# Kernel tuning notes

Hardware: AMD Instinct MI355X
Metric: run time of the kernel (lower is better)

## Reference

```python
import math
import jax, jax.numpy as jnp
import numpy as np

B, S, D, H = 4, 2048, 1024, 16

def setup_inputs() -> dict:
    key = jax.random.key(0)
    k1, k2, k3 = jax.random.split(key, 3)
    scale_in = 1.0 / math.sqrt(D)
    return {
        "x": jax.random.normal(k1, (B, S, D), dtype=jnp.float32),
        "w_in": jax.random.normal(k2, (D, 3 * D), dtype=jnp.float32) * scale_in,
        "b_in": jnp.zeros((3 * D,), dtype=jnp.float32),
        "w_out": jax.random.normal(k3, (D, D), dtype=jnp.float32) * scale_in,
        "b_out": jnp.zeros((D,), dtype=jnp.float32),
    }

def reference(x, w_in, b_in, w_out, b_out):
    b, s, d = x.shape
    hd = d // H  # head dim
    qkv = x @ w_in + b_in                       # [B,S,3D]
    q, k, v = jnp.split(qkv, 3, axis=-1)        # each [B,S,D]
    # [B,H,S,hd]
    q = q.reshape(b, s, H, hd).transpose(0, 2, 1, 3)
    k = k.reshape(b, s, H, hd).transpose(0, 2, 1, 3)
    v = v.reshape(b, s, H, hd).transpose(0, 2, 1, 3)
    attn = jnp.einsum('bhqd,bhkd->bhqk', q, k) / math.sqrt(hd)  # [B,H,S,S]
    causal = jnp.tril(jnp.ones((s, s), dtype=bool))
    attn = jnp.where(causal[None, None], attn, -jnp.inf)
    attn = jax.nn.softmax(attn, axis=-1)
    out = jnp.einsum('bhqk,bhkd->bhqd', attn, v)  # [B,H,S,hd]
    out = out.transpose(0, 2, 1, 3).reshape(b, s, d)
    return out @ w_out + b_out
```

## Files before the change

kernel.cpp:

```cpp
#include <hip/hip_runtime.h>
#include <stdint.h>

#define B_   4
#define S_   2048
#define D_   1024
#define H_   16
#define HD_  64
#define BH_  (B_*H_)
#define M_   (B_*S_)
#define KD_  1024

typedef __bf16 bf16x8 __attribute__((ext_vector_type(8)));
typedef float f32x4 __attribute__((ext_vector_type(4)));
typedef float f32x16 __attribute__((ext_vector_type(16)));
typedef unsigned int u32x4 __attribute__((ext_vector_type(4)));

__device__ __forceinline__ unsigned short f2bf(float f) {
  unsigned int u = __float_as_uint(f);
  u = u + 0x7fffu + ((u >> 16) & 1u);
  return (unsigned short)(u >> 16);
}

__device__ __forceinline__ void gload16(const void* g, void* lds) {
  __builtin_amdgcn_global_load_lds(
      (__attribute__((address_space(1))) void*)(g),
      (__attribute__((address_space(3))) void*)(lds),
      16, 0, 0);
}

__device__ __forceinline__ bf16x8 ldfrag(const unsigned short* p) {
  return *reinterpret_cast<const bf16x8*>(p);
}

__device__ __forceinline__ unsigned int cvtpk(float lo, float hi) {
  unsigned int r;
  asm("v_cvt_pk_bf16_f32 %0, %1, %2" : "=v"(r) : "v"(lo), "v"(hi));
  return r;
}

__device__ __forceinline__ void plswap(unsigned int& a, unsigned int& b) {
  asm("v_permlane32_swap_b32 %0, %1" : "+v"(a), "+v"(b));
}

__device__ __forceinline__ float2 pkadd2(float2 a, float2 b) {
  float2 r;
  asm("v_pk_add_f32 %0, %1, %2" : "=v"(r) : "v"(a), "v"(b));
  return r;
}

__device__ __forceinline__ bf16x8 mkfrag(unsigned int a, unsigned int b,
                                         unsigned int c, unsigned int d) {
  union { unsigned int w[4]; bf16x8 v; } u;
  u.w[0] = a; u.w[1] = b; u.w[2] = c; u.w[3] = d;
  return u.v;
}

__global__ __launch_bounds__(256) void xconv(const float* __restrict__ in,
                                             unsigned short* __restrict__ out) {
  const size_t i = (size_t)blockIdx.x * 256 + threadIdx.x;
  const float4* p = reinterpret_cast<const float4*>(in) + i * 2;
  float4 a = p[0], b = p[1];
  union { u32x4 v; unsigned short u[8]; } cv;
  cv.u[0] = f2bf(a.x); cv.u[1] = f2bf(a.y); cv.u[2] = f2bf(a.z); cv.u[3] = f2bf(a.w);
  cv.u[4] = f2bf(b.x); cv.u[5] = f2bf(b.y); cv.u[6] = f2bf(b.z); cv.u[7] = f2bf(b.w);
  *reinterpret_cast<u32x4*>(out + i * 8) = cv.v;
}

__global__ __launch_bounds__(256) void wtrans(const float* __restrict__ src,
                                              unsigned short* __restrict__ dst,
                                              int R, int C) {
  __shared__ float t[32][33];
  const int c0 = blockIdx.x * 32, r0 = blockIdx.y * 32;
  const int x = threadIdx.x & 31, y = threadIdx.x >> 5;
#pragma unroll
  for (int yy = y; yy < 32; yy += 8)
    t[yy][x] = src[(size_t)(r0 + yy) * C + c0 + x];
  __syncthreads();
#pragma unroll
  for (int yy = y; yy < 32; yy += 8)
    dst[(size_t)(c0 + yy) * R + r0 + x] = f2bf(t[x][yy]);
}

__global__ __launch_bounds__(256) void qkv_gemm(
    const unsigned short* __restrict__ A,
    const unsigned short* __restrict__ Bt,
    const float* __restrict__ bias,
    unsigned short* __restrict__ Qo,
    unsigned short* __restrict__ Ko,
    unsigned short* __restrict__ Vto)
{
  __shared__ unsigned short Al[2][128 * 32];
  __shared__ unsigned short Bl[2][128 * 32];
  const int tid = threadIdx.x;
  const int w = tid >> 6, l = tid & 63;
  const int g = l >> 4, c = l & 15;
  const int m0 = blockIdx.y * 128, n0 = blockIdx.x * 128;
  const int wr = (w >> 1) * 64, wc = (w & 1) * 64;

  f32x4 acc[4][4] = {};

  const int srow = w * 32 + (l >> 2);
  const int slc  = ((l & 3) ^ ((l >> 3) & 3)) * 8;
  const unsigned short* Ag = A  + (size_t)(m0 + srow) * KD_ + slc;
  const unsigned short* Bg = Bt + (size_t)(n0 + srow) * KD_ + slc;

  const int sA = (c >> 1) & 3;

#define GSTAGE(buf, kt) do {                                    \
    gload16(Ag + (kt),            &Al[buf][(w*32)*32]);         \
    gload16(Ag + 16*KD_ + (kt),   &Al[buf][(w*32+16)*32]);      \
    gload16(Bg + (kt),            &Bl[buf][(w*32)*32]);         \
    gload16(Bg + 16*KD_ + (kt),   &Bl[buf][(w*32+16)*32]);      \
  } while (0)

  GSTAGE(0, 0);
  int cur = 0;
  for (int kt = 0; kt < KD_; kt += 32) {
    if (kt + 32 < KD_) {
      GSTAGE(cur ^ 1, kt + 32);
      asm volatile("s_waitcnt vmcnt(4)" ::: "memory");
    } else {
      asm volatile("s_waitcnt vmcnt(0)" ::: "memory");
    }
    __builtin_amdgcn_s_barrier();
    __builtin_amdgcn_sched_barrier(0);
    bf16x8 af[4], bfr[4];
#pragma unroll
    for (int i = 0; i < 4; ++i)
      af[i] = ldfrag(&Al[cur][(wr + i * 16 + c) * 32 + ((g ^ sA) << 3)]);
#pragma unroll
    for (int j = 0; j < 4; ++j)
      bfr[j] = ldfrag(&Bl[cur][(wc + j * 16 + c) * 32 + ((g ^ sA) << 3)]);
#pragma unroll
    for (int i = 0; i < 4; ++i)
#pragma unroll
      for (int j = 0; j < 4; ++j)
        acc[i][j] = __builtin_amdgcn_mfma_f32_16x16x32_bf16(af[i], bfr[j], acc[i][j], 0, 0, 0);
    __builtin_amdgcn_sched_barrier(0);
    __builtin_amdgcn_s_barrier();
    cur ^= 1;
  }
#undef GSTAGE

  if (n0 >= 2048) {
#pragma unroll
    for (int i = 0; i < 4; ++i)
#pragma unroll
      for (int j = 0; j < 4; ++j) {
        const int ng = n0 + wc + j * 16 + c;
        const int n  = ng - 2048;
        const int hh = n >> 6, dim = n & 63;
        const int m  = m0 + wr + i * 16 + g * 4;
        const int bb = m >> 11, ss = m & 2047;
        const float bv = bias[ng];
        uint2 pk;
        pk.x = cvtpk(acc[i][j][0] + bv, acc[i][j][1] + bv);
        pk.y = cvtpk(acc[i][j][2] + bv, acc[i][j][3] + bv);
        *reinterpret_cast<uint2*>(
            &Vto[((size_t)(bb * H_ + hh) * HD_ + dim) * S_ + ss]) = pk;
      }
  } else {
#pragma unroll
    for (int i = 0; i < 4; ++i)
#pragma unroll
      for (int j = 0; j < 4; ++j)
#pragma unroll
        for (int r = 0; r < 4; ++r) {
          const int m = m0 + wr + i * 16 + g * 4 + r;
          const int n = n0 + wc + j * 16 + c;
          float v = acc[i][j][r] + bias[n];
          const int which = n >> 10;
          const int dp = n & 1023;
          const int hh = dp >> 6, dim = dp & 63;
          const int bb = m >> 11, ss = m & 2047;
          const size_t idx = ((size_t)(bb * H_ + hh) * S_ + ss) * HD_ + dim;
          if (which == 0) Qo[idx] = f2bf(v * 0.18033688f);
          else            Ko[idx] = f2bf(v);
        }
  }
}

__global__ __launch_bounds__(256) void out_gemm(
    const unsigned short* __restrict__ A,
    const unsigned short* __restrict__ Bt,
    const float* __restrict__ bias,
    float* __restrict__ C)
{
  __shared__ unsigned short Al[2][128 * 32];
  __shared__ unsigned short Bl[2][128 * 32];
  const int tid = threadIdx.x;
  const int w = tid >> 6, l = tid & 63;
  const int g = l >> 4, c = l & 15;
  const int m0 = blockIdx.y * 128, n0 = blockIdx.x * 128;
  const int wr = (w >> 1) * 64, wc = (w & 1) * 64;

  f32x4 acc[4][4] = {};

  const int srow = w * 32 + (l >> 2);
  const int slc  = ((l & 3) ^ ((l >> 3) & 3)) * 8;
  const unsigned short* Ag = A  + (size_t)(m0 + srow) * KD_ + slc;
  const unsigned short* Bg = Bt + (size_t)(n0 + srow) * KD_ + slc;

  const int sA = (c >> 1) & 3;

#define GSTAGE(buf, kt) do {                                    \
    gload16(Ag + (kt),            &Al[buf][(w*32)*32]);         \
    gload16(Ag + 16*KD_ + (kt),   &Al[buf][(w*32+16)*32]);      \
    gload16(Bg + (kt),            &Bl[buf][(w*32)*32]);         \
    gload16(Bg + 16*KD_ + (kt),   &Bl[buf][(w*32+16)*32]);      \
  } while (0)

  GSTAGE(0, 0);
  int cur = 0;
  for (int kt = 0; kt < KD_; kt += 32) {
    if (kt + 32 < KD_) {
      GSTAGE(cur ^ 1, kt + 32);
      asm volatile("s_waitcnt vmcnt(4)" ::: "memory");
    } else {
      asm volatile("s_waitcnt vmcnt(0)" ::: "memory");
    }
    __builtin_amdgcn_s_barrier();
    __builtin_amdgcn_sched_barrier(0);
    bf16x8 af[4], bfr[4];
#pragma unroll
    for (int i = 0; i < 4; ++i)
      af[i] = ldfrag(&Al[cur][(wr + i * 16 + c) * 32 + ((g ^ sA) << 3)]);
#pragma unroll
    for (int j = 0; j < 4; ++j)
      bfr[j] = ldfrag(&Bl[cur][(wc + j * 16 + c) * 32 + ((g ^ sA) << 3)]);
#pragma unroll
    for (int i = 0; i < 4; ++i)
#pragma unroll
      for (int j = 0; j < 4; ++j)
        acc[i][j] = __builtin_amdgcn_mfma_f32_16x16x32_bf16(af[i], bfr[j], acc[i][j], 0, 0, 0);
    __builtin_amdgcn_sched_barrier(0);
    __builtin_amdgcn_s_barrier();
    cur ^= 1;
  }
#undef GSTAGE

#pragma unroll
  for (int i = 0; i < 4; ++i)
#pragma unroll
    for (int j = 0; j < 4; ++j)
#pragma unroll
      for (int r = 0; r < 4; ++r) {
        const int m = m0 + wr + i * 16 + g * 4 + r;
        const int n = n0 + wc + j * 16 + c;
        C[(size_t)m * D_ + n] = acc[i][j][r] + bias[n];
      }
}

__global__ __launch_bounds__(256) void attn_fwd4(
    const unsigned short* __restrict__ Q,
    const unsigned short* __restrict__ Kg,
    const unsigned short* __restrict__ Vt,
    unsigned short* __restrict__ O)
{
  __shared__ unsigned short Kl[2][64 * 64];
  __shared__ unsigned short Vl[2][64 * 64];

  const int tid = threadIdx.x;
  const int w = tid >> 6, l = tid & 63;
  const int q32 = l & 31, hi = l >> 5;

  const int raw = blockIdx.y * 8 + blockIdx.x;
  const int work = (raw & 7) * 64 + (raw >> 3);
  const int bh = work >> 3;
  const int p  = work & 7;
  const int q0A = p * 128;
  const int q0B = (15 - p) * 128;
  const int nA = 2 * (p + 1);
  const int nB = 2 * (16 - p);
  const int total = nA + nB;

  const unsigned short* Kbh = Kg + (size_t)bh * (S_ * HD_);
  const unsigned short* Vbh = Vt + (size_t)bh * (HD_ * S_);

  bf16x8 qf[4];
  auto loadQ = [&](int q0) {
    const unsigned short* Qrow = Q + ((size_t)bh * S_ + q0 + w * 32 + q32) * HD_ + hi * 8;
#pragma unroll
    for (int s = 0; s < 4; ++s) qf[s] = ldfrag(Qrow + s * 16);
  };

  f32x16 od0 = {}, od1 = {};
  float lrun = 0.f;

  const int krow = w * 16 + (l >> 3);
  const int slc = ((l & 7) ^ (l >> 3)) * 8;

#define LDSOFF(r, ch) ((r) * 64 + (((ch) ^ ((r) & 7)) << 3))

#define STAGE(buf, tile) do {                                                   \
    const int k0s = (tile) * 64;                                                \
    gload16(Kbh + (size_t)(k0s + krow) * HD_ + slc,     &Kl[buf][(w*16)*64]);   \
    gload16(Kbh + (size_t)(k0s + krow + 8) * HD_ + slc, &Kl[buf][(w*16+8)*64]); \
    gload16(Vbh + (size_t)krow * S_ + k0s + slc,        &Vl[buf][(w*16)*64]);   \
    gload16(Vbh + (size_t)(krow + 8) * S_ + k0s + slc,  &Vl[buf][(w*16+8)*64]); \
  } while (0)

  auto epilogue = [&](int q0) {
    const float rl = 1.0f / lrun;
    const int bb = bh >> 4, hh = bh & 15;
    const int sq = q0 + w * 32 + q32;
    unsigned short* Orow = O + ((size_t)bb * S_ + sq) * D_ + hh * HD_;
#pragma unroll
    for (int rr = 0; rr < 4; ++rr) {
      uint2 v0, v1;
      v0.x = cvtpk(od0[4 * rr] * rl,     od0[4 * rr + 1] * rl);
      v0.y = cvtpk(od0[4 * rr + 2] * rl, od0[4 * rr + 3] * rl);
      *reinterpret_cast<uint2*>(Orow + 8 * rr + 4 * hi) = v0;
      v1.x = cvtpk(od1[4 * rr] * rl,     od1[4 * rr + 1] * rl);
      v1.y = cvtpk(od1[4 * rr + 2] * rl, od1[4 * rr + 3] * rl);
      *reinterpret_cast<uint2*>(Orow + 32 + 8 * rr + 4 * hi) = v1;
    }
  };

  loadQ(q0A);
  STAGE(0, 0);
  int cur = 0;
  int q0 = q0A;

  for (int idx = 0; idx < total; ++idx) {
    const bool inA = idx < nA;
    const int kv = inA ? idx : idx - nA;
    const int k0 = kv * 64;
    if (idx + 1 < total) {
      const int nkv = (idx + 1 < nA) ? idx + 1 : idx + 1 - nA;
      STAGE(cur ^ 1, nkv);
      asm volatile("s_waitcnt vmcnt(4)" ::: "memory");
    } else {
      asm volatile("s_waitcnt vmcnt(0)" ::: "memory");
    }
    __builtin_amdgcn_s_barrier();
    __builtin_amdgcn_sched_barrier(0);

    const int wqmin = q0 + w * 32;
    if (k0 <= wqmin + 31) {
      const bool live1 = (k0 + 32 <= wqmin + 31);
      const unsigned short* Kb_ = &Kl[cur][0];
      const unsigned short* Vb_ = &Vl[cur][0];

      f32x16 st0 = {}, st1 = {};
      __builtin_amdgcn_s_setprio(1);
#pragma unroll
      for (int s = 0; s < 4; ++s) {
        bf16x8 kf = ldfrag(Kb_ + LDSOFF(q32, 2 * s + hi));
        st0 = __builtin_amdgcn_mfma_f32_32x32x16_bf16(kf, qf[s], st0, 0, 0, 0);
      }
      if (live1) {
#pragma unroll
        for (int s = 0; s < 4; ++s) {
          bf16x8 kf = ldfrag(Kb_ + LDSOFF(32 + q32, 2 * s + hi));
          st1 = __builtin_amdgcn_mfma_f32_32x32x16_bf16(kf, qf[s], st1, 0, 0, 0);
        }
      }
      __builtin_amdgcn_s_setprio(0);

      if (k0 + 63 > wqmin) {
        const int rel = wqmin + q32 - k0;
#pragma unroll
        for (int r = 0; r < 16; ++r) {
          const int kva = (r & 3) + 8 * (r >> 2) + 4 * hi;
          if (kva > rel) st0[r] = -1e30f;
        }
        if (live1) {
#pragma unroll
          for (int r = 0; r < 16; ++r) {
            const int kva = (r & 3) + 8 * (r >> 2) + 4 * hi;
            if (kva + 32 > rel) st1[r] = -1e30f;
          }
        }
      }

      float2 e0[8], e1[8];
#pragma unroll
      for (int r = 0; r < 8; ++r) {
        e0[r].x = __builtin_amdgcn_exp2f(st0[2 * r]);
        e0[r].y = __builtin_amdgcn_exp2f(st0[2 * r + 1]);
      }
      float2 a0 = pkadd2(pkadd2(e0[0], e0[1]), pkadd2(e0[2], e0[3]));
      float2 a1 = pkadd2(pkadd2(e0[4], e0[5]), pkadd2(e0[6], e0[7]));
      float2 asum = pkadd2(a0, a1);
      if (live1) {
#pragma unroll
        for (int r = 0; r < 8; ++r) {
          e1[r].x = __builtin_amdgcn_exp2f(st1[2 * r]);
          e1[r].y = __builtin_amdgcn_exp2f(st1[2 * r + 1]);
        }
        float2 b0 = pkadd2(pkadd2(e1[0], e1[1]), pkadd2(e1[2], e1[3]));
        float2 b1 = pkadd2(pkadd2(e1[4], e1[5]), pkadd2(e1[6], e1[7]));
        asum = pkadd2(asum, pkadd2(b0, b1));
      }
      float ps = asum.x + asum.y;
      ps += __shfl_xor(ps, 32);
      lrun += ps;

      unsigned int W0, W1, W2, W3, W4, W5, W6, W7;
      W0 = cvtpk(e0[0].x, e0[0].y); W1 = cvtpk(e0[1].x, e0[1].y);
      W2 = cvtpk(e0[2].x, e0[2].y); W3 = cvtpk(e0[3].x, e0[3].y);
      W4 = cvtpk(e0[4].x, e0[4].y); W5 = cvtpk(e0[5].x, e0[5].y);
      W6 = cvtpk(e0[6].x, e0[6].y); W7 = cvtpk(e0[7].x, e0[7].y);
      plswap(W0, W2); plswap(W1, W3); plswap(W4, W6); plswap(W5, W7);
      const bf16x8 pa0 = mkfrag(W0, W1, W2, W3);
      const bf16x8 pa1 = mkfrag(W4, W5, W6, W7);
      bf16x8 pa2, pa3;
      if (live1) {
        W0 = cvtpk(e1[0].x, e1[0].y); W1 = cvtpk(e1[1].x, e1[1].y);
        W2 = cvtpk(e1[2].x, e1[2].y); W3 = cvtpk(e1[3].x, e1[3].y);
        W4 = cvtpk(e1[4].x, e1[4].y); W5 = cvtpk(e1[5].x, e1[5].y);
        W6 = cvtpk(e1[6].x, e1[6].y); W7 = cvtpk(e1[7].x, e1[7].y);
        plswap(W0, W2); plswap(W1, W3); plswap(W4, W6); plswap(W5, W7);
        pa2 = mkfrag(W0, W1, W2, W3);
        pa3 = mkfrag(W4, W5, W6, W7);
      }

      __builtin_amdgcn_s_setprio(1);
#pragma unroll
      for (int s = 0; s < 2; ++s) {
        const bf16x8 pa = (s == 0) ? pa0 : pa1;
        bf16x8 vf = ldfrag(Vb_ + LDSOFF(q32, 2 * s + hi));
        od0 = __builtin_amdgcn_mfma_f32_32x32x16_bf16(vf, pa, od0, 0, 0, 0);
        bf16x8 vg = ldfrag(Vb_ + LDSOFF(32 + q32, 2 * s + hi));
        od1 = __builtin_amdgcn_mfma_f32_32x32x16_bf16(vg, pa, od1, 0, 0, 0);
      }
      if (live1) {
#pragma unroll
        for (int s = 2; s < 4; ++s) {
          const bf16x8 pa = (s == 2) ? pa2 : pa3;
          bf16x8 vf = ldfrag(Vb_ + LDSOFF(q32, 2 * s + hi));
          od0 = __builtin_amdgcn_mfma_f32_32x32x16_bf16(vf, pa, od0, 0, 0, 0);
          bf16x8 vg = ldfrag(Vb_ + LDSOFF(32 + q32, 2 * s + hi));
          od1 = __builtin_amdgcn_mfma_f32_32x32x16_bf16(vg, pa, od1, 0, 0, 0);
        }
      }
      __builtin_amdgcn_s_setprio(0);
    }

    __builtin_amdgcn_sched_barrier(0);
    __builtin_amdgcn_s_barrier();

    if (idx == nA - 1) {
      epilogue(q0A);
      loadQ(q0B);
      od0 = {}; od1 = {};
      lrun = 0.f;
      q0 = q0B;
    }
    cur ^= 1;
  }

  epilogue(q0B);
#undef STAGE
#undef LDSOFF
}

extern "C" void kernel_launch(void* const* d_in, const int* in_sizes, int n_in,
                              void* d_out, int out_size, void* d_ws, size_t ws_size,
                              hipStream_t stream) {
  (void)in_sizes; (void)n_in; (void)out_size; (void)ws_size;
  const float* x     = (const float*)d_in[0];
  const float* w_in  = (const float*)d_in[1];
  const float* b_in  = (const float*)d_in[2];
  const float* w_out = (const float*)d_in[3];
  const float* b_out = (const float*)d_in[4];
  float* out = (float*)d_out;
  char* ws = (char*)d_ws;
  const size_t MB = 1024 * 1024;
  unsigned short* xb     = (unsigned short*)(ws);
  unsigned short* w_inb  = (unsigned short*)(ws + 16 * MB);
  unsigned short* w_outb = (unsigned short*)(ws + 22 * MB);
  unsigned short* Qb     = (unsigned short*)(ws + 24 * MB);
  unsigned short* Kb     = (unsigned short*)(ws + 40 * MB);
  unsigned short* Vt     = (unsigned short*)(ws + 56 * MB);
  unsigned short* Ob     = (unsigned short*)(ws + 72 * MB);

  xconv<<<4096, 256, 0, stream>>>(x, xb);
  wtrans<<<dim3(96, 32), 256, 0, stream>>>(w_in, w_inb, 1024, 3072);
  wtrans<<<dim3(32, 32), 256, 0, stream>>>(w_out, w_outb, 1024, 1024);
  qkv_gemm<<<dim3(24, 64), 256, 0, stream>>>(xb, w_inb, b_in, Qb, Kb, Vt);
  attn_fwd4<<<dim3(8, 64), 256, 0, stream>>>(Qb, Kb, Vt, Ob);
  out_gemm<<<dim3(8, 64), 256, 0, stream>>>(Ob, w_outb, b_out, out);
}
```

Before: 172.1 us.

## Deepen GEMM to 4-stage and attention to 3-stage LDS pipelines

Both GEMMs now use a 4-buffer LDS ring with three K tiles prefetched, and the main loop is fully unrolled with per-iteration vmcnt waits. The trailing barrier is dropped, so each iteration needs only one barrier. The attention kernel moves from double to triple buffering: it prefetches two KV tiles ahead, issues the next load after the barrier and also drops the trailing barrier. This is meant to hide more global-load latency and cut synchronisation, at the cost of twice the GEMM LDS (64KB per block) and 1.5x the attention LDS, which may lower occupancy.

```diff
diff --git a/kernel.cpp b/kernel.cpp
--- a/kernel.cpp
+++ b/kernel.cpp
@@ -81,6 +81,36 @@
     dst[(size_t)(c0 + yy) * R + r0 + x] = f2bf(t[x][yy]);
 }
 
+#define GSTAGE(buf, kt) do {                                    \
+    gload16(Ag + (kt),            &Al[buf][(w*32)*32]);         \
+    gload16(Ag + 16*KD_ + (kt),   &Al[buf][(w*32+16)*32]);      \
+    gload16(Bg + (kt),            &Bl[buf][(w*32)*32]);         \
+    gload16(Bg + 16*KD_ + (kt),   &Bl[buf][(w*32+16)*32]);      \
+  } while (0)
+
+#define GEMM_ITER(T_, VM_)                                                    \
+  {                                                                           \
+    asm volatile("s_waitcnt vmcnt(" VM_ ")" ::: "memory");                    \
+    __builtin_amdgcn_s_barrier();                                             \
+    __builtin_amdgcn_sched_barrier(0);                                        \
+    if ((T_) + 3 < 32) GSTAGE(((T_) + 3) & 3, ((T_) + 3) * 32);               \
+    const unsigned short* Ab_ = &Al[(T_) & 3][0];                             \
+    const unsigned short* Bb_ = &Bl[(T_) & 3][0];                             \
+    bf16x8 af[4], bfr[4];                                                     \
+    _Pragma("unroll")                                                         \
+    for (int i_ = 0; i_ < 4; ++i_)                                            \
+      af[i_] = ldfrag(&Ab_[(wr + i_ * 16 + c) * 32 + ((g ^ sA) << 3)]);       \
+    _Pragma("unroll")                                                         \
+    for (int j_ = 0; j_ < 4; ++j_)                                            \
+      bfr[j_] = ldfrag(&Bb_[(wc + j_ * 16 + c) * 32 + ((g ^ sA) << 3)]);      \
+    _Pragma("unroll")                                                         \
+    for (int i_ = 0; i_ < 4; ++i_)                                            \
+      _Pragma("unroll")                                                       \
+      for (int j_ = 0; j_ < 4; ++j_)                                          \
+        acc[i_][j_] = __builtin_amdgcn_mfma_f32_16x16x32_bf16(                \
+            af[i_], bfr[j_], acc[i_][j_], 0, 0, 0);                           \
+  }
+
 __global__ __launch_bounds__(256) void qkv_gemm(
     const unsigned short* __restrict__ A,
     const unsigned short* __restrict__ Bt,
@@ -89,8 +119,8 @@
     unsigned short* __restrict__ Ko,
     unsigned short* __restrict__ Vto)
 {
-  __shared__ unsigned short Al[2][128 * 32];
-  __shared__ unsigned short Bl[2][128 * 32];
+  __shared__ unsigned short Al[4][128 * 32];
+  __shared__ unsigned short Bl[4][128 * 32];
   const int tid = threadIdx.x;
   const int w = tid >> 6, l = tid & 63;
   const int g = l >> 4, c = l & 15;
@@ -106,41 +136,13 @@
 
   const int sA = (c >> 1) & 3;
 
-#define GSTAGE(buf, kt) do {                                    \
-    gload16(Ag + (kt),            &Al[buf][(w*32)*32]);         \
-    gload16(Ag + 16*KD_ + (kt),   &Al[buf][(w*32+16)*32]);      \
-    gload16(Bg + (kt),            &Bl[buf][(w*32)*32]);         \
-    gload16(Bg + 16*KD_ + (kt),   &Bl[buf][(w*32+16)*32]);      \
-  } while (0)
-
   GSTAGE(0, 0);
-  int cur = 0;
-  for (int kt = 0; kt < KD_; kt += 32) {
-    if (kt + 32 < KD_) {
-      GSTAGE(cur ^ 1, kt + 32);
-      asm volatile("s_waitcnt vmcnt(4)" ::: "memory");
-    } else {
-      asm volatile("s_waitcnt vmcnt(0)" ::: "memory");
-    }
-    __builtin_amdgcn_s_barrier();
-    __builtin_amdgcn_sched_barrier(0);
-    bf16x8 af[4], bfr[4];
-#pragma unroll
-    for (int i = 0; i < 4; ++i)
-      af[i] = ldfrag(&Al[cur][(wr + i * 16 + c) * 32 + ((g ^ sA) << 3)]);
-#pragma unroll
-    for (int j = 0; j < 4; ++j)
-      bfr[j] = ldfrag(&Bl[cur][(wc + j * 16 + c) * 32 + ((g ^ sA) << 3)]);
-#pragma unroll
-    for (int i = 0; i < 4; ++i)
-#pragma unroll
-      for (int j = 0; j < 4; ++j)
-        acc[i][j] = __builtin_amdgcn_mfma_f32_16x16x32_bf16(af[i], bfr[j], acc[i][j], 0, 0, 0);
-    __builtin_amdgcn_sched_barrier(0);
-    __builtin_amdgcn_s_barrier();
-    cur ^= 1;
-  }
-#undef GSTAGE
+  GSTAGE(1, 32);
+  GSTAGE(2, 64);
+  for (int t = 0; t < 29; ++t) GEMM_ITER(t, "12");
+  GEMM_ITER(29, "8");
+  GEMM_ITER(30, "4");
+  GEMM_ITER(31, "0");
 
   if (n0 >= 2048) {
 #pragma unroll
@@ -186,8 +188,8 @@
     const float* __restrict__ bias,
     float* __restrict__ C)
 {
-  __shared__ unsigned short Al[2][128 * 32];
-  __shared__ unsigned short Bl[2][128 * 32];
+  __shared__ unsigned short Al[4][128 * 32];
+  __shared__ unsigned short Bl[4][128 * 32];
   const int tid = threadIdx.x;
   const int w = tid >> 6, l = tid & 63;
   const int g = l >> 4, c = l & 15;
@@ -203,41 +205,13 @@
 
   const int sA = (c >> 1) & 3;
 
-#define GSTAGE(buf, kt) do {                                    \
-    gload16(Ag + (kt),            &Al[buf][(w*32)*32]);         \
-    gload16(Ag + 16*KD_ + (kt),   &Al[buf][(w*32+16)*32]);      \
-    gload16(Bg + (kt),            &Bl[buf][(w*32)*32]);         \
-    gload16(Bg + 16*KD_ + (kt),   &Bl[buf][(w*32+16)*32]);      \
-  } while (0)
-
   GSTAGE(0, 0);
-  int cur = 0;
-  for (int kt = 0; kt < KD_; kt += 32) {
-    if (kt + 32 < KD_) {
-      GSTAGE(cur ^ 1, kt + 32);
-      asm volatile("s_waitcnt vmcnt(4)" ::: "memory");
-    } else {
-      asm volatile("s_waitcnt vmcnt(0)" ::: "memory");
-    }
-    __builtin_amdgcn_s_barrier();
-    __builtin_amdgcn_sched_barrier(0);
-    bf16x8 af[4], bfr[4];
-#pragma unroll
-    for (int i = 0; i < 4; ++i)
-      af[i] = ldfrag(&Al[cur][(wr + i * 16 + c) * 32 + ((g ^ sA) << 3)]);
-#pragma unroll
-    for (int j = 0; j < 4; ++j)
-      bfr[j] = ldfrag(&Bl[cur][(wc + j * 16 + c) * 32 + ((g ^ sA) << 3)]);
-#pragma unroll
-    for (int i = 0; i < 4; ++i)
-#pragma unroll
-      for (int j = 0; j < 4; ++j)
-        acc[i][j] = __builtin_amdgcn_mfma_f32_16x16x32_bf16(af[i], bfr[j], acc[i][j], 0, 0, 0);
-    __builtin_amdgcn_sched_barrier(0);
-    __builtin_amdgcn_s_barrier();
-    cur ^= 1;
-  }
-#undef GSTAGE
+  GSTAGE(1, 32);
+  GSTAGE(2, 64);
+  for (int t = 0; t < 29; ++t) GEMM_ITER(t, "12");
+  GEMM_ITER(29, "8");
+  GEMM_ITER(30, "4");
+  GEMM_ITER(31, "0");
 
 #pragma unroll
   for (int i = 0; i < 4; ++i)
@@ -251,14 +225,14 @@
       }
 }
 
-__global__ __launch_bounds__(256) void attn_fwd4(
+__global__ __launch_bounds__(256) void attn_fwd5(
     const unsigned short* __restrict__ Q,
     const unsigned short* __restrict__ Kg,
     const unsigned short* __restrict__ Vt,
     unsigned short* __restrict__ O)
 {
-  __shared__ unsigned short Kl[2][64 * 64];
-  __shared__ unsigned short Vl[2][64 * 64];
+  __shared__ unsigned short Kl[3][64 * 64];
+  __shared__ unsigned short Vl[3][64 * 64];
 
   const int tid = threadIdx.x;
   const int w = tid >> 6, l = tid & 63;
@@ -271,8 +245,6 @@
   const int q0A = p * 128;
   const int q0B = (15 - p) * 128;
   const int nA = 2 * (p + 1);
-  const int nB = 2 * (16 - p);
-  const int total = nA + nB;
 
   const unsigned short* Kbh = Kg + (size_t)bh * (S_ * HD_);
   const unsigned short* Vbh = Vt + (size_t)bh * (HD_ * S_);
@@ -319,22 +291,24 @@
 
   loadQ(q0A);
   STAGE(0, 0);
+  STAGE(1, 1);
   int cur = 0;
   int q0 = q0A;
 
-  for (int idx = 0; idx < total; ++idx) {
-    const bool inA = idx < nA;
-    const int kv = inA ? idx : idx - nA;
+  for (int idx = 0; idx < 34; ++idx) {
+    const int kv = (idx < nA) ? idx : idx - nA;
     const int k0 = kv * 64;
-    if (idx + 1 < total) {
-      const int nkv = (idx + 1 < nA) ? idx + 1 : idx + 1 - nA;
-      STAGE(cur ^ 1, nkv);
-      asm volatile("s_waitcnt vmcnt(4)" ::: "memory");
-    } else {
-      asm volatile("s_waitcnt vmcnt(0)" ::: "memory");
-    }
+    if (idx != 33) asm volatile("s_waitcnt vmcnt(4)" ::: "memory");
+    else           asm volatile("s_waitcnt vmcnt(0)" ::: "memory");
     __builtin_amdgcn_s_barrier();
     __builtin_amdgcn_sched_barrier(0);
+
+    if (idx + 2 < 34) {
+      const int i2 = idx + 2;
+      const int nkv = (i2 < nA) ? i2 : i2 - nA;
+      int sb = cur + 2; if (sb >= 3) sb -= 3;
+      STAGE(sb, nkv);
+    }
 
     const int wqmin = q0 + w * 32;
     if (k0 <= wqmin + 31) {
@@ -438,9 +412,6 @@
       __builtin_amdgcn_s_setprio(0);
     }
 
-    __builtin_amdgcn_sched_barrier(0);
-    __builtin_amdgcn_s_barrier();
-
     if (idx == nA - 1) {
       epilogue(q0A);
       loadQ(q0B);
@@ -448,7 +419,7 @@
       lrun = 0.f;
       q0 = q0B;
     }
-    cur ^= 1;
+    cur = (cur == 2) ? 0 : cur + 1;
   }
 
   epilogue(q0B);
@@ -480,6 +451,6 @@
   wtrans<<<dim3(96, 32), 256, 0, stream>>>(w_in, w_inb, 1024, 3072);
   wtrans<<<dim3(32, 32), 256, 0, stream>>>(w_out, w_outb, 1024, 1024);
   qkv_gemm<<<dim3(24, 64), 256, 0, stream>>>(xb, w_inb, b_in, Qb, Kb, Vt);
-  attn_fwd4<<<dim3(8, 64), 256, 0, stream>>>(Qb, Kb, Vt, Ob);
+  attn_fwd5<<<dim3(8, 64), 256, 0, stream>>>(Qb, Kb, Vt, Ob);
   out_gemm<<<dim3(8, 64), 256, 0, stream>>>(Ob, w_outb, b_out, out);
 }
```

After: 184.4 us. 1.07x slower.

## Fuse fp32-to-bf16 conversion of x into QKV GEMM A-tile loading

Applied to the files above, without the earlier changes.

Drops the separate xconv kernel and has qkv_gemm read fp32 x directly, converting to bf16 in registers and writing packed values into LDS. This removes one kernel launch and a full round trip of the bf16 copy of x through memory. In exchange the A operand now goes through registers rather than direct global-to-LDS loads, and each block re-reads fp32 x, twice the bytes, for each of the 24 column tiles. The pipeline also switches to a full vmcnt(0) wait every iteration, which can reduce latency hiding.

```diff
diff --git a/kernel.cpp b/kernel.cpp
--- a/kernel.cpp
+++ b/kernel.cpp
@@ -55,17 +55,6 @@
   return u.v;
 }
 
-__global__ __launch_bounds__(256) void xconv(const float* __restrict__ in,
-                                             unsigned short* __restrict__ out) {
-  const size_t i = (size_t)blockIdx.x * 256 + threadIdx.x;
-  const float4* p = reinterpret_cast<const float4*>(in) + i * 2;
-  float4 a = p[0], b = p[1];
-  union { u32x4 v; unsigned short u[8]; } cv;
-  cv.u[0] = f2bf(a.x); cv.u[1] = f2bf(a.y); cv.u[2] = f2bf(a.z); cv.u[3] = f2bf(a.w);
-  cv.u[4] = f2bf(b.x); cv.u[5] = f2bf(b.y); cv.u[6] = f2bf(b.z); cv.u[7] = f2bf(b.w);
-  *reinterpret_cast<u32x4*>(out + i * 8) = cv.v;
-}
-
 __global__ __launch_bounds__(256) void wtrans(const float* __restrict__ src,
                                               unsigned short* __restrict__ dst,
                                               int R, int C) {
@@ -82,7 +71,7 @@
 }
 
 __global__ __launch_bounds__(256) void qkv_gemm(
-    const unsigned short* __restrict__ A,
+    const float* __restrict__ Af,
     const unsigned short* __restrict__ Bt,
     const float* __restrict__ bias,
     unsigned short* __restrict__ Qo,
@@ -100,30 +89,52 @@
   f32x4 acc[4][4] = {};
 
   const int srow = w * 32 + (l >> 2);
-  const int slc  = ((l & 3) ^ ((l >> 3) & 3)) * 8;
-  const unsigned short* Ag = A  + (size_t)(m0 + srow) * KD_ + slc;
-  const unsigned short* Bg = Bt + (size_t)(n0 + srow) * KD_ + slc;
+  const int lc   = l & 3;
+  const int pch  = lc ^ ((l >> 3) & 3);
+  const float* Ag0 = Af + (size_t)(m0 + srow) * KD_ + lc * 8;
+  const float* Ag1 = Ag0 + (size_t)16 * KD_;
+  const unsigned short* Bg = Bt + (size_t)(n0 + srow) * KD_ + pch * 8;
+  const int aw0 = srow * 32 + pch * 8;
+  const int aw1 = (srow + 16) * 32 + pch * 8;
 
   const int sA = (c >> 1) & 3;
 
-#define GSTAGE(buf, kt) do {                                    \
-    gload16(Ag + (kt),            &Al[buf][(w*32)*32]);         \
-    gload16(Ag + 16*KD_ + (kt),   &Al[buf][(w*32+16)*32]);      \
-    gload16(Bg + (kt),            &Bl[buf][(w*32)*32]);         \
-    gload16(Bg + 16*KD_ + (kt),   &Bl[buf][(w*32+16)*32]);      \
+#define APACK(dstbuf, off, v0, v1) do {                         \
+    u32x4 pk_;                                                  \
+    pk_[0] = cvtpk((v0).x, (v0).y); pk_[1] = cvtpk((v0).z, (v0).w); \
+    pk_[2] = cvtpk((v1).x, (v1).y); pk_[3] = cvtpk((v1).z, (v1).w); \
+    *reinterpret_cast<u32x4*>(&Al[dstbuf][off]) = pk_;          \
   } while (0)
 
-  GSTAGE(0, 0);
-  int cur = 0;
-  for (int kt = 0; kt < KD_; kt += 32) {
-    if (kt + 32 < KD_) {
-      GSTAGE(cur ^ 1, kt + 32);
-      asm volatile("s_waitcnt vmcnt(4)" ::: "memory");
-    } else {
-      asm volatile("s_waitcnt vmcnt(0)" ::: "memory");
-    }
+  {
+    float4 a00 = *reinterpret_cast<const float4*>(Ag0);
+    float4 a01 = *reinterpret_cast<const float4*>(Ag0 + 4);
+    float4 a10 = *reinterpret_cast<const float4*>(Ag1);
+    float4 a11 = *reinterpret_cast<const float4*>(Ag1 + 4);
+    gload16(Bg,             &Bl[0][(w * 32) * 32]);
+    gload16(Bg + 16 * KD_,  &Bl[0][(w * 32 + 16) * 32]);
+    APACK(0, aw0, a00, a01);
+    APACK(0, aw1, a10, a11);
+  }
+
+#pragma unroll
+  for (int t = 0; t < 32; ++t) {
+    const int cur = t & 1, nxt = cur ^ 1;
+    asm volatile("s_waitcnt vmcnt(0) lgkmcnt(0)" ::: "memory");
     __builtin_amdgcn_s_barrier();
     __builtin_amdgcn_sched_barrier(0);
+
+    float4 a00, a01, a10, a11;
+    if (t + 1 < 32) {
+      const int kt = (t + 1) * 32;
+      a00 = *reinterpret_cast<const float4*>(Ag0 + kt);
+      a01 = *reinterpret_cast<const float4*>(Ag0 + kt + 4);
+      a10 = *reinterpret_cast<const float4*>(Ag1 + kt);
+      a11 = *reinterpret_cast<const float4*>(Ag1 + kt + 4);
+      gload16(Bg + kt,            &Bl[nxt][(w * 32) * 32]);
+      gload16(Bg + 16 * KD_ + kt, &Bl[nxt][(w * 32 + 16) * 32]);
+    }
+
     bf16x8 af[4], bfr[4];
 #pragma unroll
     for (int i = 0; i < 4; ++i)
@@ -136,11 +147,13 @@
 #pragma unroll
       for (int j = 0; j < 4; ++j)
         acc[i][j] = __builtin_amdgcn_mfma_f32_16x16x32_bf16(af[i], bfr[j], acc[i][j], 0, 0, 0);
-    __builtin_amdgcn_sched_barrier(0);
-    __builtin_amdgcn_s_barrier();
-    cur ^= 1;
+
+    if (t + 1 < 32) {
+      APACK(nxt, aw0, a00, a01);
+      APACK(nxt, aw1, a10, a11);
+    }
   }
-#undef GSTAGE
+#undef APACK
 
   if (n0 >= 2048) {
 #pragma unroll
@@ -468,18 +481,16 @@
   float* out = (float*)d_out;
   char* ws = (char*)d_ws;
   const size_t MB = 1024 * 1024;
-  unsigned short* xb     = (unsigned short*)(ws);
-  unsigned short* w_inb  = (unsigned short*)(ws + 16 * MB);
-  unsigned short* w_outb = (unsigned short*)(ws + 22 * MB);
-  unsigned short* Qb     = (unsigned short*)(ws + 24 * MB);
-  unsigned short* Kb     = (unsigned short*)(ws + 40 * MB);
-  unsigned short* Vt     = (unsigned short*)(ws + 56 * MB);
-  unsigned short* Ob     = (unsigned short*)(ws + 72 * MB);
-
-  xconv<<<4096, 256, 0, stream>>>(x, xb);
+  unsigned short* w_inb  = (unsigned short*)(ws);
+  unsigned short* w_outb = (unsigned short*)(ws + 6 * MB);
+  unsigned short* Qb     = (unsigned short*)(ws + 8 * MB);
+  unsigned short* Kb     = (unsigned short*)(ws + 24 * MB);
+  unsigned short* Vt     = (unsigned short*)(ws + 40 * MB);
+  unsigned short* Ob     = (unsigned short*)(ws + 56 * MB);
+
   wtrans<<<dim3(96, 32), 256, 0, stream>>>(w_in, w_inb, 1024, 3072);
   wtrans<<<dim3(32, 32), 256, 0, stream>>>(w_out, w_outb, 1024, 1024);
-  qkv_gemm<<<dim3(24, 64), 256, 0, stream>>>(xb, w_inb, b_in, Qb, Kb, Vt);
+  qkv_gemm<<<dim3(24, 64), 256, 0, stream>>>(x, w_inb, b_in, Qb, Kb, Vt);
   attn_fwd4<<<dim3(8, 64), 256, 0, stream>>>(Qb, Kb, Vt, Ob);
   out_gemm<<<dim3(8, 64), 256, 0, stream>>>(Ob, w_outb, b_out, out);
 }
```

Result: slower. 186.2 us (+8.2%).

## Enlarge QKV GEMM to 256x256 tiles with 8 waves and phased pipeline

Applied to the files above, without the earlier changes.

The QKV projection GEMM now runs 512 threads per block on 256x256 output tiles with a K step of 64. It uses a swizzled double-buffered LDS layout. The K loop is split into four sub-phases, each issuing part of the next tile's global-to-LDS loads, and MFMA runs at raised wave priority. This is meant to increase operand reuse per LDS load and overlap memory traffic with matrix math. In exchange it uses about 128KB of LDS per block, so occupancy drops to one block per CU, and the grid shrinks to 384 blocks, which can leave an uneven final wave across CUs.

```diff
diff --git a/kernel.cpp b/kernel.cpp
--- a/kernel.cpp
+++ b/kernel.cpp
@@ -81,7 +81,7 @@
     dst[(size_t)(c0 + yy) * R + r0 + x] = f2bf(t[x][yy]);
 }
 
-__global__ __launch_bounds__(256) void qkv_gemm(
+__global__ __launch_bounds__(512, 2) void qkv_gemm8(
     const unsigned short* __restrict__ A,
     const unsigned short* __restrict__ Bt,
     const float* __restrict__ bias,
@@ -89,86 +89,123 @@
     unsigned short* __restrict__ Ko,
     unsigned short* __restrict__ Vto)
 {
-  __shared__ unsigned short Al[2][128 * 32];
-  __shared__ unsigned short Bl[2][128 * 32];
+  __shared__ unsigned short As[2][2][128 * 64];
+  __shared__ unsigned short Bs[2][2][128 * 64];
+
   const int tid = threadIdx.x;
   const int w = tid >> 6, l = tid & 63;
-  const int g = l >> 4, c = l & 15;
-  const int m0 = blockIdx.y * 128, n0 = blockIdx.x * 128;
-  const int wr = (w >> 1) * 64, wc = (w & 1) * 64;
-
-  f32x4 acc[4][4] = {};
-
-  const int srow = w * 32 + (l >> 2);
-  const int slc  = ((l & 3) ^ ((l >> 3) & 3)) * 8;
-  const unsigned short* Ag = A  + (size_t)(m0 + srow) * KD_ + slc;
-  const unsigned short* Bg = Bt + (size_t)(n0 + srow) * KD_ + slc;
-
-  const int sA = (c >> 1) & 3;
-
-#define GSTAGE(buf, kt) do {                                    \
-    gload16(Ag + (kt),            &Al[buf][(w*32)*32]);         \
-    gload16(Ag + 16*KD_ + (kt),   &Al[buf][(w*32+16)*32]);      \
-    gload16(Bg + (kt),            &Bl[buf][(w*32)*32]);         \
-    gload16(Bg + 16*KD_ + (kt),   &Bl[buf][(w*32+16)*32]);      \
+  const int c = l & 15, g = l >> 4;
+  const int wm = w >> 2, wn = w & 3;
+  const int m0 = blockIdx.y * 256, n0 = blockIdx.x * 256;
+
+  f32x4 acc[8][4] = {};
+
+  const int srow = w * 8 + (l >> 3);
+  const int schunk = ((l & 7) ^ ((w * 4 + (l >> 4)) & 7)) * 8;
+  const unsigned short* Asrc = A  + (size_t)(m0 + srow) * KD_ + schunk;
+  const unsigned short* Bsrc = Bt + (size_t)(n0 + srow) * KD_ + schunk;
+  const int ldst = (w * 8) * 64;
+
+#define STAGE_A(b_, kt_) do {                                              \
+    gload16(Asrc + (kt_) * 64,                     &As[b_][0][ldst]);      \
+    gload16(Asrc + (size_t)64  * KD_ + (kt_) * 64, &As[b_][0][ldst + 4096]); \
+    gload16(Asrc + (size_t)128 * KD_ + (kt_) * 64, &As[b_][1][ldst]);      \
+    gload16(Asrc + (size_t)192 * KD_ + (kt_) * 64, &As[b_][1][ldst + 4096]); \
   } while (0)
-
-  GSTAGE(0, 0);
-  int cur = 0;
-  for (int kt = 0; kt < KD_; kt += 32) {
-    if (kt + 32 < KD_) {
-      GSTAGE(cur ^ 1, kt + 32);
-      asm volatile("s_waitcnt vmcnt(4)" ::: "memory");
+#define STAGE_B(b_, kt_) do {                                              \
+    gload16(Bsrc + (kt_) * 64,                     &Bs[b_][0][ldst]);      \
+    gload16(Bsrc + (size_t)64  * KD_ + (kt_) * 64, &Bs[b_][0][ldst + 4096]); \
+    gload16(Bsrc + (size_t)128 * KD_ + (kt_) * 64, &Bs[b_][1][ldst]);      \
+    gload16(Bsrc + (size_t)192 * KD_ + (kt_) * 64, &Bs[b_][1][ldst + 4096]); \
+  } while (0)
+
+  const int sw = c >> 1;
+
+#define PHASE(BUF_, QM_, QN_, STAGING_, TAILWAIT_)                          \
+  {                                                                         \
+    bf16x8 af[4][2], bfr[2][2];                                             \
+    _Pragma("unroll")                                                       \
+    for (int i_ = 0; i_ < 4; ++i_) {                                        \
+      const int rA = (QM_) * 64 + i_ * 16 + c;                              \
+      _Pragma("unroll")                                                     \
+      for (int ks = 0; ks < 2; ++ks)                                        \
+        af[i_][ks] = ldfrag(&As[BUF_][wm][rA * 64 + (((ks << 2) + g) ^ sw) * 8]); \
+    }                                                                       \
+    _Pragma("unroll")                                                       \
+    for (int j_ = 0; j_ < 2; ++j_) {                                        \
+      const int rB = (wn & 1) * 64 + (QN_) * 32 + j_ * 16 + c;              \
+      _Pragma("unroll")                                                     \
+      for (int ks = 0; ks < 2; ++ks)                                        \
+        bfr[j_][ks] = ldfrag(&Bs[BUF_][wn >> 1][rB * 64 + (((ks << 2) + g) ^ sw) * 8]); \
+    }                                                                       \
+    STAGING_                                                                \
+    __builtin_amdgcn_s_barrier();                                           \
+    asm volatile("s_waitcnt lgkmcnt(0)" ::: "memory");                      \
+    __builtin_amdgcn_sched_barrier(0);                                      \
+    __builtin_amdgcn_s_setprio(1);                                          \
+    _Pragma("unroll")                                                       \
+    for (int i_ = 0; i_ < 4; ++i_)                                          \
+      _Pragma("unroll")                                                     \
+      for (int j_ = 0; j_ < 2; ++j_)                                        \
+        _Pragma("unroll")                                                   \
+        for (int ks = 0; ks < 2; ++ks)                                      \
+          acc[(QM_) * 4 + i_][(QN_) * 2 + j_] =                             \
+              __builtin_amdgcn_mfma_f32_16x16x32_bf16(                      \
+                  af[i_][ks], bfr[j_][ks],                                  \
+                  acc[(QM_) * 4 + i_][(QN_) * 2 + j_], 0, 0, 0);            \
+    __builtin_amdgcn_s_setprio(0);                                          \
+    TAILWAIT_                                                               \
+    __builtin_amdgcn_s_barrier();                                           \
+  }
+
+  STAGE_A(0, 0);
+  STAGE_B(0, 0);
+  asm volatile("s_waitcnt vmcnt(0)" ::: "memory");
+  __builtin_amdgcn_s_barrier();
+
+  for (int kt = 0; kt < 16; ++kt) {
+    const int buf = kt & 1;
+    if (kt < 15) {
+      PHASE(buf, 0, 0, STAGE_A(buf ^ 1, kt + 1);, )
+      PHASE(buf, 1, 0, STAGE_B(buf ^ 1, kt + 1);, )
     } else {
-      asm volatile("s_waitcnt vmcnt(0)" ::: "memory");
+      PHASE(buf, 0, 0, , )
+      PHASE(buf, 1, 0, , )
     }
-    __builtin_amdgcn_s_barrier();
-    __builtin_amdgcn_sched_barrier(0);
-    bf16x8 af[4], bfr[4];
-#pragma unroll
-    for (int i = 0; i < 4; ++i)
-      af[i] = ldfrag(&Al[cur][(wr + i * 16 + c) * 32 + ((g ^ sA) << 3)]);
-#pragma unroll
-    for (int j = 0; j < 4; ++j)
-      bfr[j] = ldfrag(&Bl[cur][(wc + j * 16 + c) * 32 + ((g ^ sA) << 3)]);
-#pragma unroll
-    for (int i = 0; i < 4; ++i)
-#pragma unroll
-      for (int j = 0; j < 4; ++j)
-        acc[i][j] = __builtin_amdgcn_mfma_f32_16x16x32_bf16(af[i], bfr[j], acc[i][j], 0, 0, 0);
-    __builtin_amdgcn_sched_barrier(0);
-    __builtin_amdgcn_s_barrier();
-    cur ^= 1;
+    PHASE(buf, 0, 1, , )
+    PHASE(buf, 1, 1, , asm volatile("s_waitcnt vmcnt(0)" ::: "memory");)
   }
-#undef GSTAGE
+#undef PHASE
+#undef STAGE_A
+#undef STAGE_B
 
   if (n0 >= 2048) {
 #pragma unroll
-    for (int i = 0; i < 4; ++i)
-#pragma unroll
-      for (int j = 0; j < 4; ++j) {
-        const int ng = n0 + wc + j * 16 + c;
-        const int n  = ng - 2048;
-        const int hh = n >> 6, dim = n & 63;
-        const int m  = m0 + wr + i * 16 + g * 4;
+    for (int mi = 0; mi < 8; ++mi)
+#pragma unroll
+      for (int nj = 0; nj < 4; ++nj) {
+        const int ng = n0 + wn * 64 + nj * 16 + c;
+        const int nn = ng - 2048;
+        const int hh = nn >> 6, dim = nn & 63;
+        const int m  = m0 + wm * 128 + mi * 16 + g * 4;
         const int bb = m >> 11, ss = m & 2047;
         const float bv = bias[ng];
         uint2 pk;
-        pk.x = cvtpk(acc[i][j][0] + bv, acc[i][j][1] + bv);
-        pk.y = cvtpk(acc[i][j][2] + bv, acc[i][j][3] + bv);
+        pk.x = cvtpk(acc[mi][nj][0] + bv, acc[mi][nj][1] + bv);
+        pk.y = cvtpk(acc[mi][nj][2] + bv, acc[mi][nj][3] + bv);
         *reinterpret_cast<uint2*>(
             &Vto[((size_t)(bb * H_ + hh) * HD_ + dim) * S_ + ss]) = pk;
       }
   } else {
 #pragma unroll
-    for (int i = 0; i < 4; ++i)
-#pragma unroll
-      for (int j = 0; j < 4; ++j)
+    for (int mi = 0; mi < 8; ++mi)
+#pragma unroll
+      for (int nj = 0; nj < 4; ++nj)
 #pragma unroll
         for (int r = 0; r < 4; ++r) {
-          const int m = m0 + wr + i * 16 + g * 4 + r;
-          const int n = n0 + wc + j * 16 + c;
-          float v = acc[i][j][r] + bias[n];
+          const int m = m0 + wm * 128 + mi * 16 + g * 4 + r;
+          const int n = n0 + wn * 64 + nj * 16 + c;
+          float v = acc[mi][nj][r] + bias[n];
           const int which = n >> 10;
           const int dp = n & 1023;
           const int hh = dp >> 6, dim = dp & 63;
@@ -479,7 +516,7 @@
   xconv<<<4096, 256, 0, stream>>>(x, xb);
   wtrans<<<dim3(96, 32), 256, 0, stream>>>(w_in, w_inb, 1024, 3072);
   wtrans<<<dim3(32, 32), 256, 0, stream>>>(w_out, w_outb, 1024, 1024);
-  qkv_gemm<<<dim3(24, 64), 256, 0, stream>>>(xb, w_inb, b_in, Qb, Kb, Vt);
+  qkv_gemm8<<<dim3(12, 32), 512, 0, stream>>>(xb, w_inb, b_in, Qb, Kb, Vt);
   attn_fwd4<<<dim3(8, 64), 256, 0, stream>>>(Qb, Kb, Vt, Ob);
   out_gemm<<<dim3(8, 64), 256, 0, stream>>>(Ob, w_outb, b_out, out);
 }
```

Measured after the change: 183.8 us. 1.07x slower.
